# Performance work log

Measured on AMD Instinct MI355X. Metric: run time of the kernel, lower is better.

The kernel has to match this reference:

```python
import jax, jax.numpy as jnp
import numpy as np

N = 100000   # nodes
E = 5000000  # edges (avg degree 50)
H = 16       # hidden dim


def gcn_conv(x, edge_index, edge_weight, W, b, num_nodes):
    """PyG GCNConv with edge weights: add self-loops (weight 1), symmetric
    normalization deg^-1/2 * w * deg^-1/2, linear transform, scatter-add."""
    row, col = edge_index[0], edge_index[1]  # source j -> target i
    loop = jnp.arange(num_nodes, dtype=edge_index.dtype)
    row = jnp.concatenate([row, loop])
    col = jnp.concatenate([col, loop])
    w = jnp.concatenate([edge_weight, jnp.ones((num_nodes,), edge_weight.dtype)])
    deg = jax.ops.segment_sum(w, col, num_segments=num_nodes)
    dinv = jnp.where(deg > 0, jax.lax.rsqrt(jnp.where(deg > 0, deg, 1.0)), 0.0)
    norm = dinv[row] * w * dinv[col]               # [E+N]
    h = x @ W                                      # [N, out]
    msg = norm[:, None] * h[row]                   # gather + scale
    out = jax.ops.segment_sum(msg, col, num_segments=num_nodes)  # scatter-add
    return out + b


def setup_inputs() -> dict:
    key = jax.random.key(0)
    k = jax.random.split(key, 7)
    x = jax.random.normal(k[0], (N, 1), dtype=jnp.float32)
    edge_index = jax.random.randint(k[1], (2, E), 0, N, dtype=jnp.int32)
    edge_attr = jax.random.uniform(k[2], (E,), dtype=jnp.float32)
    W1 = jax.random.normal(k[3], (1, H), dtype=jnp.float32) * (1.0 / np.sqrt(1.0))
    b1 = jnp.zeros((H,), dtype=jnp.float32)
    W2 = jax.random.normal(k[4], (H, 1), dtype=jnp.float32) * (1.0 / np.sqrt(H))
    b2 = jnp.zeros((1,), dtype=jnp.float32)
    return {"x": x, "edge_index": edge_index, "edge_attr": edge_attr,
            "W1": W1, "b1": b1, "W2": W2, "b2": b2}


def reference(x, edge_index, edge_attr, W1, b1, W2, b2):
    h = gcn_conv(x, edge_index, edge_attr, W1, b1, N)
    h = jax.nn.relu(h)
    out = gcn_conv(h, edge_index, edge_attr, W2, b2, N)
    return out
```

## Files before the change

kernel.cpp:

```cpp
#include <hip/hip_runtime.h>

#define T       256
#define BSHIFT  12
#define BSIZE   4096
#define MAXNB   32
#define MM      48
#define EPB     2048
#define EPT     (EPB / T)
#define CAP     212992

typedef int   i4 __attribute__((ext_vector_type(4)));
typedef int   i2 __attribute__((ext_vector_type(2)));
typedef float f4 __attribute__((ext_vector_type(4)));

__global__ __launch_bounds__(T) void k_scatter(
        const int* __restrict__ row, const int* __restrict__ col,
        const float* __restrict__ w, int* __restrict__ gcnt,
        i2* __restrict__ rec, int E, int nb) {
    __shared__ i2  buf[EPB];
    __shared__ int rnk[MAXNB];
    __shared__ int lofs[MAXNB + 1];
    __shared__ int rbase[MAXNB];
    int t = threadIdx.x, g = blockIdx.x;
    if (t < MAXNB) rnk[t] = 0;
    __syncthreads();
    int base = g * EPB;
    bool full = (base + EPB <= E);
    i4 c0, c1;
    if (full) {
        c0 = __builtin_nontemporal_load((const i4*)(col + base + (t + 0 * T) * 4));
        c1 = __builtin_nontemporal_load((const i4*)(col + base + (t + 1 * T) * 4));
        atomicAdd(&rnk[c0.x >> BSHIFT], 1); atomicAdd(&rnk[c0.y >> BSHIFT], 1);
        atomicAdd(&rnk[c0.z >> BSHIFT], 1); atomicAdd(&rnk[c0.w >> BSHIFT], 1);
        atomicAdd(&rnk[c1.x >> BSHIFT], 1); atomicAdd(&rnk[c1.y >> BSHIFT], 1);
        atomicAdd(&rnk[c1.z >> BSHIFT], 1); atomicAdd(&rnk[c1.w >> BSHIFT], 1);
    } else {
        for (int k = 0; k < EPT; ++k) {
            int e = base + t + k * T;
            if (e < E) atomicAdd(&rnk[col[e] >> BSHIFT], 1);
        }
    }
    __syncthreads();
    if (t < 64) {
        int v = (t < nb) ? rnk[t] : 0;
        int inc = v;
#pragma unroll
        for (int d = 1; d < 32; d <<= 1) {
            int o = __shfl_up(inc, d, 64);
            if (t >= d) inc += o;
        }
        if (t == 0) lofs[0] = 0;
        if (t < nb) {
            lofs[t + 1] = inc;
            rbase[t] = t * CAP + atomicAdd(&gcnt[t], v);
        }
    }
    __syncthreads();
    if (t < MAXNB) rnk[t] = 0;
    __syncthreads();
    auto place = [&](int c, int r, float wv) {
        int b = c >> BSHIFT;
        int pos = lofs[b] + atomicAdd(&rnk[b], 1);
        i2 v;
        v.x = ((c & (BSIZE - 1)) << 17) | r;
        v.y = __float_as_int(wv);
        buf[pos] = v;
    };
    if (full) {
        {
            int idx = base + (t + 0 * T) * 4;
            i4 r  = __builtin_nontemporal_load((const i4*)(row + idx));
            f4 wv = __builtin_nontemporal_load((const f4*)(w + idx));
            place(c0.x, r.x, wv.x); place(c0.y, r.y, wv.y);
            place(c0.z, r.z, wv.z); place(c0.w, r.w, wv.w);
        }
        {
            int idx = base + (t + 1 * T) * 4;
            i4 r  = __builtin_nontemporal_load((const i4*)(row + idx));
            f4 wv = __builtin_nontemporal_load((const f4*)(w + idx));
            place(c1.x, r.x, wv.x); place(c1.y, r.y, wv.y);
            place(c1.z, r.z, wv.z); place(c1.w, r.w, wv.w);
        }
    } else {
        for (int k = 0; k < EPT; ++k) {
            int e = base + t + k * T;
            if (e < E) place(col[e], row[e], w[e]);
        }
    }
    __syncthreads();
    int total = lofs[nb];
    int b = 0;
    for (int j = t; j < total; j += T) {
        while (j >= lofs[b + 1]) ++b;
        __builtin_nontemporal_store(buf[j], &rec[rbase[b] + (j - lofs[b])]);
    }
}

template <bool HAS_SRC>
__global__ __launch_bounds__(T) void k_acc(
        const i2* __restrict__ rec, const int* __restrict__ gcnt,
        const float* __restrict__ src, float* __restrict__ part) {
    __shared__ float acc[BSIZE];
    int t = threadIdx.x, g = blockIdx.x;
    int b = g / MM, m = g % MM;
    f4* acc4 = (f4*)acc;
    for (int j = t; j < BSIZE / 4; j += T) acc4[j] = (f4){0.f, 0.f, 0.f, 0.f};
    __syncthreads();
    int s0 = b * CAP;
    int tb = gcnt[b];
    int chunk = ((tb + MM - 1) / MM + 7) & ~7;
    int lo = s0 + m * chunk;
    int hi = min(s0 + tb, lo + chunk);
    const i4* rec4 = (const i4*)rec;
    int i = lo + t * 8;
    for (; i + 7 < hi; i += T * 8) {
        i4 q0 = __builtin_nontemporal_load(rec4 + (i >> 1) + 0);
        i4 q1 = __builtin_nontemporal_load(rec4 + (i >> 1) + 1);
        i4 q2 = __builtin_nontemporal_load(rec4 + (i >> 1) + 2);
        i4 q3 = __builtin_nontemporal_load(rec4 + (i >> 1) + 3);
        float v0 = __int_as_float(q0.y), v1 = __int_as_float(q0.w);
        float v2 = __int_as_float(q1.y), v3 = __int_as_float(q1.w);
        float v4 = __int_as_float(q2.y), v5 = __int_as_float(q2.w);
        float v6 = __int_as_float(q3.y), v7 = __int_as_float(q3.w);
        if (HAS_SRC) {
            v0 *= src[q0.x & 0x1FFFF]; v1 *= src[q0.z & 0x1FFFF];
            v2 *= src[q1.x & 0x1FFFF]; v3 *= src[q1.z & 0x1FFFF];
            v4 *= src[q2.x & 0x1FFFF]; v5 *= src[q2.z & 0x1FFFF];
            v6 *= src[q3.x & 0x1FFFF]; v7 *= src[q3.z & 0x1FFFF];
        }
        atomicAdd(&acc[((unsigned)q0.x) >> 17], v0);
        atomicAdd(&acc[((unsigned)q0.z) >> 17], v1);
        atomicAdd(&acc[((unsigned)q1.x) >> 17], v2);
        atomicAdd(&acc[((unsigned)q1.z) >> 17], v3);
        atomicAdd(&acc[((unsigned)q2.x) >> 17], v4);
        atomicAdd(&acc[((unsigned)q2.z) >> 17], v5);
        atomicAdd(&acc[((unsigned)q3.x) >> 17], v6);
        atomicAdd(&acc[((unsigned)q3.z) >> 17], v7);
    }
    for (; i < hi; ++i) {
        i2 r = rec[i];
        float v = __int_as_float(r.y);
        if (HAS_SRC) v *= src[r.x & 0x1FFFF];
        atomicAdd(&acc[((unsigned)r.x) >> 17], v);
    }
    __syncthreads();
    f4* dst4 = (f4*)(part + (size_t)g * BSIZE);
    for (int j = t; j < BSIZE / 4; j += T)
        __builtin_nontemporal_store(acc4[j], dst4 + j);
}

__device__ __forceinline__ float reduceM(const float* __restrict__ part, int n) {
    int b = n >> BSHIFT, o = n & (BSIZE - 1);
    const float* pp = part + (size_t)b * MM * BSIZE + o;
    float s = 0.0f;
#pragma unroll
    for (int m = 0; m < MM; ++m) s += pp[(size_t)m * BSIZE];
    return s;
}

__global__ void k_red_dinv(const float* __restrict__ part, const float* __restrict__ x,
                           float* __restrict__ dinv, float* __restrict__ p, int N) {
    int i = blockIdx.x * blockDim.x + threadIdx.x;
    if (i < N) {
        float d  = reduceM(part, i) + 1.0f;
        float di = rsqrtf(d);
        dinv[i] = di;
        p[i] = di * x[i];
    }
}

__global__ void k_red_mlp(const float* __restrict__ part, const float* __restrict__ dinv,
                          const float* __restrict__ p,
                          const float* __restrict__ W1, const float* __restrict__ b1,
                          const float* __restrict__ W2,
                          float* __restrict__ q, int N) {
    int i = blockIdx.x * blockDim.x + threadIdx.x;
    if (i < N) {
        float di = dinv[i];
        float s  = di * reduceM(part, i) + di * p[i];
        float acc = 0.0f;
#pragma unroll
        for (int k = 0; k < 16; ++k) {
            float h = fmaxf(s * W1[k] + b1[k], 0.0f);
            acc += h * W2[k];
        }
        q[i] = di * acc;
    }
}

__global__ void k_red_out(const float* __restrict__ part, const float* __restrict__ dinv,
                          const float* __restrict__ q, const float* __restrict__ b2,
                          float* __restrict__ out, int N) {
    int i = blockIdx.x * blockDim.x + threadIdx.x;
    if (i < N) {
        float di = dinv[i];
        out[i] = di * reduceM(part, i) + di * q[i] + b2[0];
    }
}

extern "C" void kernel_launch(void* const* d_in, const int* in_sizes, int n_in,
                              void* d_out, int out_size, void* d_ws, size_t ws_size,
                              hipStream_t stream) {
    const float* x  = (const float*)d_in[0];
    const int*   ei = (const int*)  d_in[1];
    const float* ew = (const float*)d_in[2];
    const float* W1 = (const float*)d_in[3];
    const float* b1 = (const float*)d_in[4];
    const float* W2 = (const float*)d_in[5];
    const float* b2 = (const float*)d_in[6];

    const int N = in_sizes[0];
    const int E = in_sizes[2];
    const int* row = ei;
    const int* col = ei + E;
    const int nb = (N + BSIZE - 1) >> BSHIFT;
    const int eb = (E + EPB - 1) / EPB;

    char* wsp = (char*)d_ws;
    auto take = [&](size_t bytes) {
        char* r = wsp; wsp += (bytes + 255) & ~(size_t)255; return (void*)r;
    };
    i2*    rec  = (i2*)   take((size_t)nb * CAP * 8);
    float* part = (float*)take((size_t)nb * MM * BSIZE * 4);
    float* dinv = (float*)take((size_t)N * 4);
    float* p    = (float*)take((size_t)N * 4);
    float* q    = (float*)take((size_t)N * 4);
    int*   gcnt = (int*)  take(MAXNB * 4);

    float* out = (float*)d_out;

    const int nbk = (N + T - 1) / T;
    const int ab  = nb * MM;

    (void)hipMemsetAsync(gcnt, 0, MAXNB * sizeof(int), stream);

    k_scatter<<<eb, T, 0, stream>>>(row, col, ew, gcnt, rec, E, nb);

    k_acc<false><<<ab, T, 0, stream>>>(rec, gcnt, nullptr, part);
    k_red_dinv  <<<nbk, T, 0, stream>>>(part, x, dinv, p, N);

    k_acc<true><<<ab, T, 0, stream>>>(rec, gcnt, p, part);
    k_red_mlp  <<<nbk, T, 0, stream>>>(part, dinv, p, W1, b1, W2, q, N);

    k_acc<true><<<ab, T, 0, stream>>>(rec, gcnt, q, part);
    k_red_out  <<<nbk, T, 0, stream>>>(part, dinv, q, b2, out, N);
}
```

Measured before the change: 256.8 us.

## Replace bucketed LDS scatter with direct global float atomics per edge pass

Drops the bucketing pre-pass, the per-bucket LDS accumulation and the partial-sum reduction. Each pass now streams row/col/w and does unsafeAtomicAdd straight into global per-node arrays (deg, s1, s2), which are zeroed by one memset. This removes the 40 MB record write/read and the partial buffers, but sends 5M global float atomics per pass to random addresses in a 400 KB array. The edge arrays are now read three times instead of once. Summation order becomes nondeterministic.

```diff
diff --git a/kernel.cpp b/kernel.cpp
--- a/kernel.cpp
+++ b/kernel.cpp
@@ -1,183 +1,87 @@
 #include <hip/hip_runtime.h>
 
-#define T       256
-#define BSHIFT  12
-#define BSIZE   4096
-#define MAXNB   32
-#define MM      48
-#define EPB     2048
-#define EPT     (EPB / T)
-#define CAP     212992
+#define T    256
+#define EPB  2048
+#define NPAD 102400
 
 typedef int   i4 __attribute__((ext_vector_type(4)));
-typedef int   i2 __attribute__((ext_vector_type(2)));
 typedef float f4 __attribute__((ext_vector_type(4)));
 
-__global__ __launch_bounds__(T) void k_scatter(
-        const int* __restrict__ row, const int* __restrict__ col,
-        const float* __restrict__ w, int* __restrict__ gcnt,
-        i2* __restrict__ rec, int E, int nb) {
-    __shared__ i2  buf[EPB];
-    __shared__ int rnk[MAXNB];
-    __shared__ int lofs[MAXNB + 1];
-    __shared__ int rbase[MAXNB];
-    int t = threadIdx.x, g = blockIdx.x;
-    if (t < MAXNB) rnk[t] = 0;
-    __syncthreads();
-    int base = g * EPB;
-    bool full = (base + EPB <= E);
-    i4 c0, c1;
-    if (full) {
-        c0 = __builtin_nontemporal_load((const i4*)(col + base + (t + 0 * T) * 4));
-        c1 = __builtin_nontemporal_load((const i4*)(col + base + (t + 1 * T) * 4));
-        atomicAdd(&rnk[c0.x >> BSHIFT], 1); atomicAdd(&rnk[c0.y >> BSHIFT], 1);
-        atomicAdd(&rnk[c0.z >> BSHIFT], 1); atomicAdd(&rnk[c0.w >> BSHIFT], 1);
-        atomicAdd(&rnk[c1.x >> BSHIFT], 1); atomicAdd(&rnk[c1.y >> BSHIFT], 1);
-        atomicAdd(&rnk[c1.z >> BSHIFT], 1); atomicAdd(&rnk[c1.w >> BSHIFT], 1);
-    } else {
-        for (int k = 0; k < EPT; ++k) {
-            int e = base + t + k * T;
-            if (e < E) atomicAdd(&rnk[col[e] >> BSHIFT], 1);
-        }
-    }
-    __syncthreads();
-    if (t < 64) {
-        int v = (t < nb) ? rnk[t] : 0;
-        int inc = v;
+__device__ __forceinline__ void gadd(float* a, float v) {
+    unsafeAtomicAdd(a, v);
+}
+
+__global__ __launch_bounds__(T) void k_deg(const int* __restrict__ col,
+                                           const float* __restrict__ w,
+                                           float* __restrict__ deg, int E) {
+    int t = threadIdx.x;
+    long base = (long)blockIdx.x * EPB;
+    if (base + EPB <= E) {
 #pragma unroll
-        for (int d = 1; d < 32; d <<= 1) {
-            int o = __shfl_up(inc, d, 64);
-            if (t >= d) inc += o;
-        }
-        if (t == 0) lofs[0] = 0;
-        if (t < nb) {
-            lofs[t + 1] = inc;
-            rbase[t] = t * CAP + atomicAdd(&gcnt[t], v);
-        }
-    }
-    __syncthreads();
-    if (t < MAXNB) rnk[t] = 0;
-    __syncthreads();
-    auto place = [&](int c, int r, float wv) {
-        int b = c >> BSHIFT;
-        int pos = lofs[b] + atomicAdd(&rnk[b], 1);
-        i2 v;
-        v.x = ((c & (BSIZE - 1)) << 17) | r;
-        v.y = __float_as_int(wv);
-        buf[pos] = v;
-    };
-    if (full) {
-        {
-            int idx = base + (t + 0 * T) * 4;
-            i4 r  = __builtin_nontemporal_load((const i4*)(row + idx));
+        for (int k = 0; k < 2; ++k) {
+            long idx = base + (t + k * T) * 4;
+            i4 c  = __builtin_nontemporal_load((const i4*)(col + idx));
             f4 wv = __builtin_nontemporal_load((const f4*)(w + idx));
-            place(c0.x, r.x, wv.x); place(c0.y, r.y, wv.y);
-            place(c0.z, r.z, wv.z); place(c0.w, r.w, wv.w);
-        }
-        {
-            int idx = base + (t + 1 * T) * 4;
-            i4 r  = __builtin_nontemporal_load((const i4*)(row + idx));
-            f4 wv = __builtin_nontemporal_load((const f4*)(w + idx));
-            place(c1.x, r.x, wv.x); place(c1.y, r.y, wv.y);
-            place(c1.z, r.z, wv.z); place(c1.w, r.w, wv.w);
+            gadd(&deg[c.x], wv.x);
+            gadd(&deg[c.y], wv.y);
+            gadd(&deg[c.z], wv.z);
+            gadd(&deg[c.w], wv.w);
         }
     } else {
-        for (int k = 0; k < EPT; ++k) {
-            int e = base + t + k * T;
-            if (e < E) place(col[e], row[e], w[e]);
+        for (int k = 0; k < 8; ++k) {
+            long e = base + t + k * T;
+            if (e < E) gadd(&deg[col[e]], w[e]);
         }
-    }
-    __syncthreads();
-    int total = lofs[nb];
-    int b = 0;
-    for (int j = t; j < total; j += T) {
-        while (j >= lofs[b + 1]) ++b;
-        __builtin_nontemporal_store(buf[j], &rec[rbase[b] + (j - lofs[b])]);
     }
 }
 
-template <bool HAS_SRC>
-__global__ __launch_bounds__(T) void k_acc(
-        const i2* __restrict__ rec, const int* __restrict__ gcnt,
-        const float* __restrict__ src, float* __restrict__ part) {
-    __shared__ float acc[BSIZE];
-    int t = threadIdx.x, g = blockIdx.x;
-    int b = g / MM, m = g % MM;
-    f4* acc4 = (f4*)acc;
-    for (int j = t; j < BSIZE / 4; j += T) acc4[j] = (f4){0.f, 0.f, 0.f, 0.f};
-    __syncthreads();
-    int s0 = b * CAP;
-    int tb = gcnt[b];
-    int chunk = ((tb + MM - 1) / MM + 7) & ~7;
-    int lo = s0 + m * chunk;
-    int hi = min(s0 + tb, lo + chunk);
-    const i4* rec4 = (const i4*)rec;
-    int i = lo + t * 8;
-    for (; i + 7 < hi; i += T * 8) {
-        i4 q0 = __builtin_nontemporal_load(rec4 + (i >> 1) + 0);
-        i4 q1 = __builtin_nontemporal_load(rec4 + (i >> 1) + 1);
-        i4 q2 = __builtin_nontemporal_load(rec4 + (i >> 1) + 2);
-        i4 q3 = __builtin_nontemporal_load(rec4 + (i >> 1) + 3);
-        float v0 = __int_as_float(q0.y), v1 = __int_as_float(q0.w);
-        float v2 = __int_as_float(q1.y), v3 = __int_as_float(q1.w);
-        float v4 = __int_as_float(q2.y), v5 = __int_as_float(q2.w);
-        float v6 = __int_as_float(q3.y), v7 = __int_as_float(q3.w);
-        if (HAS_SRC) {
-            v0 *= src[q0.x & 0x1FFFF]; v1 *= src[q0.z & 0x1FFFF];
-            v2 *= src[q1.x & 0x1FFFF]; v3 *= src[q1.z & 0x1FFFF];
-            v4 *= src[q2.x & 0x1FFFF]; v5 *= src[q2.z & 0x1FFFF];
-            v6 *= src[q3.x & 0x1FFFF]; v7 *= src[q3.z & 0x1FFFF];
+__global__ __launch_bounds__(T) void k_mp(const int* __restrict__ row,
+                                          const int* __restrict__ col,
+                                          const float* __restrict__ w,
+                                          const float* __restrict__ src,
+                                          float* __restrict__ dst, int E) {
+    int t = threadIdx.x;
+    long base = (long)blockIdx.x * EPB;
+    if (base + EPB <= E) {
+#pragma unroll
+        for (int k = 0; k < 2; ++k) {
+            long idx = base + (t + k * T) * 4;
+            i4 c  = __builtin_nontemporal_load((const i4*)(col + idx));
+            i4 r  = __builtin_nontemporal_load((const i4*)(row + idx));
+            f4 wv = __builtin_nontemporal_load((const f4*)(w + idx));
+            gadd(&dst[c.x], wv.x * src[r.x]);
+            gadd(&dst[c.y], wv.y * src[r.y]);
+            gadd(&dst[c.z], wv.z * src[r.z]);
+            gadd(&dst[c.w], wv.w * src[r.w]);
         }
-        atomicAdd(&acc[((unsigned)q0.x) >> 17], v0);
-        atomicAdd(&acc[((unsigned)q0.z) >> 17], v1);
-        atomicAdd(&acc[((unsigned)q1.x) >> 17], v2);
-        atomicAdd(&acc[((unsigned)q1.z) >> 17], v3);
-        atomicAdd(&acc[((unsigned)q2.x) >> 17], v4);
-        atomicAdd(&acc[((unsigned)q2.z) >> 17], v5);
-        atomicAdd(&acc[((unsigned)q3.x) >> 17], v6);
-        atomicAdd(&acc[((unsigned)q3.z) >> 17], v7);
+    } else {
+        for (int k = 0; k < 8; ++k) {
+            long e = base + t + k * T;
+            if (e < E) gadd(&dst[col[e]], w[e] * src[row[e]]);
+        }
     }
-    for (; i < hi; ++i) {
-        i2 r = rec[i];
-        float v = __int_as_float(r.y);
-        if (HAS_SRC) v *= src[r.x & 0x1FFFF];
-        atomicAdd(&acc[((unsigned)r.x) >> 17], v);
-    }
-    __syncthreads();
-    f4* dst4 = (f4*)(part + (size_t)g * BSIZE);
-    for (int j = t; j < BSIZE / 4; j += T)
-        __builtin_nontemporal_store(acc4[j], dst4 + j);
 }
 
-__device__ __forceinline__ float reduceM(const float* __restrict__ part, int n) {
-    int b = n >> BSHIFT, o = n & (BSIZE - 1);
-    const float* pp = part + (size_t)b * MM * BSIZE + o;
-    float s = 0.0f;
-#pragma unroll
-    for (int m = 0; m < MM; ++m) s += pp[(size_t)m * BSIZE];
-    return s;
-}
-
-__global__ void k_red_dinv(const float* __restrict__ part, const float* __restrict__ x,
-                           float* __restrict__ dinv, float* __restrict__ p, int N) {
+__global__ void k_dinv(const float* __restrict__ deg, const float* __restrict__ x,
+                       float* __restrict__ dinv, float* __restrict__ p, int N) {
     int i = blockIdx.x * blockDim.x + threadIdx.x;
     if (i < N) {
-        float d  = reduceM(part, i) + 1.0f;
+        float d  = deg[i] + 1.0f;
         float di = rsqrtf(d);
         dinv[i] = di;
         p[i] = di * x[i];
     }
 }
 
-__global__ void k_red_mlp(const float* __restrict__ part, const float* __restrict__ dinv,
-                          const float* __restrict__ p,
-                          const float* __restrict__ W1, const float* __restrict__ b1,
-                          const float* __restrict__ W2,
-                          float* __restrict__ q, int N) {
+__global__ void k_mlp(const float* __restrict__ s1, const float* __restrict__ dinv,
+                      const float* __restrict__ p,
+                      const float* __restrict__ W1, const float* __restrict__ b1,
+                      const float* __restrict__ W2,
+                      float* __restrict__ q, int N) {
     int i = blockIdx.x * blockDim.x + threadIdx.x;
     if (i < N) {
         float di = dinv[i];
-        float s  = di * reduceM(part, i) + di * p[i];
+        float s  = di * s1[i] + di * p[i];
         float acc = 0.0f;
 #pragma unroll
         for (int k = 0; k < 16; ++k) {
@@ -188,13 +92,13 @@
     }
 }
 
-__global__ void k_red_out(const float* __restrict__ part, const float* __restrict__ dinv,
-                          const float* __restrict__ q, const float* __restrict__ b2,
-                          float* __restrict__ out, int N) {
+__global__ void k_out(const float* __restrict__ s2, const float* __restrict__ dinv,
+                      const float* __restrict__ q, const float* __restrict__ b2,
+                      float* __restrict__ out, int N) {
     int i = blockIdx.x * blockDim.x + threadIdx.x;
     if (i < N) {
         float di = dinv[i];
-        out[i] = di * reduceM(part, i) + di * q[i] + b2[0];
+        out[i] = di * s2[i] + di * q[i] + b2[0];
     }
 }
 
@@ -213,35 +117,32 @@
     const int E = in_sizes[2];
     const int* row = ei;
     const int* col = ei + E;
-    const int nb = (N + BSIZE - 1) >> BSHIFT;
-    const int eb = (E + EPB - 1) / EPB;
 
     char* wsp = (char*)d_ws;
     auto take = [&](size_t bytes) {
         char* r = wsp; wsp += (bytes + 255) & ~(size_t)255; return (void*)r;
     };
-    i2*    rec  = (i2*)   take((size_t)nb * CAP * 8);
-    float* part = (float*)take((size_t)nb * MM * BSIZE * 4);
-    float* dinv = (float*)take((size_t)N * 4);
-    float* p    = (float*)take((size_t)N * 4);
-    float* q    = (float*)take((size_t)N * 4);
-    int*   gcnt = (int*)  take(MAXNB * 4);
+    float* zbase = (float*)take((size_t)3 * NPAD * 4);
+    float* deg   = zbase;
+    float* s1    = zbase + NPAD;
+    float* s2    = zbase + 2 * NPAD;
+    float* dinv  = (float*)take((size_t)N * 4);
+    float* p     = (float*)take((size_t)N * 4);
+    float* q     = (float*)take((size_t)N * 4);
 
     float* out = (float*)d_out;
 
+    const int ebk = (E + EPB - 1) / EPB;
     const int nbk = (N + T - 1) / T;
-    const int ab  = nb * MM;
 
-    (void)hipMemsetAsync(gcnt, 0, MAXNB * sizeof(int), stream);
+    (void)hipMemsetAsync(zbase, 0, (size_t)3 * NPAD * 4, stream);
 
-    k_scatter<<<eb, T, 0, stream>>>(row, col, ew, gcnt, rec, E, nb);
+    k_deg <<<ebk, T, 0, stream>>>(col, ew, deg, E);
+    k_dinv<<<nbk, T, 0, stream>>>(deg, x, dinv, p, N);
 
-    k_acc<false><<<ab, T, 0, stream>>>(rec, gcnt, nullptr, part);
-    k_red_dinv  <<<nbk, T, 0, stream>>>(part, x, dinv, p, N);
+    k_mp  <<<ebk, T, 0, stream>>>(row, col, ew, p, s1, E);
+    k_mlp <<<nbk, T, 0, stream>>>(s1, dinv, p, W1, b1, W2, q, N);
 
-    k_acc<true><<<ab, T, 0, stream>>>(rec, gcnt, p, part);
-    k_red_mlp  <<<nbk, T, 0, stream>>>(part, dinv, p, W1, b1, W2, q, N);
-
-    k_acc<true><<<ab, T, 0, stream>>>(rec, gcnt, q, part);
-    k_red_out  <<<nbk, T, 0, stream>>>(part, dinv, q, b2, out, N);
+    k_mp  <<<ebk, T, 0, stream>>>(row, col, ew, q, s2, E);
+    k_out <<<nbk, T, 0, stream>>>(s2, dinv, q, b2, out, N);
 }
```

Result: slower. 881.6 us (+243.4%).
